# Optimization experiments

Measured on AMD Instinct MI355X. Metric: run time of the kernel, lower is better.

## Reference

```python
import jax, jax.numpy as jnp
from jax import lax
import numpy as np

# Quantization / layer config (mirrors QuantizedConv2d init_kwargs)
IN_ZP = 3
OUT_ZP = -2
IN_SCALE = 0.05
OUT_SCALE = 0.1
STRIDE = (1, 1)
PAD = (1, 1)  # (pad_h, pad_w)
DILATION = (1, 1)
GROUPS = 1
FEATURE_BITS = 8
Q_MIN, Q_MAX = -(1 << (FEATURE_BITS - 1)), (1 << (FEATURE_BITS - 1)) - 1  # -128, 127


def setup_inputs() -> dict:
    key = jax.random.key(0)
    k1, k2, k3, k4 = jax.random.split(key, 4)
    N, Cin, H, W = 32, 128, 56, 56
    Cout, KH, KW = 256, 3, 3
    x = jax.random.randint(k1, (N, Cin, H, W), -128, 128, dtype=jnp.int8)
    weight = jax.random.randint(k2, (Cout, Cin, KH, KW), -128, 128, dtype=jnp.int8)
    bias = jax.random.randint(k3, (Cout,), -1000, 1000, dtype=jnp.int32)  # shifted quantized bias
    weight_scale = jax.random.uniform(k4, (Cout,), dtype=jnp.float32, minval=1e-3, maxval=1e-2)
    return {"x": x, "weight": weight, "bias": bias, "weight_scale": weight_scale}


def reference(x, weight, bias, weight_scale):
    # q_y = round((CONV[q_x, q_w] + shifted_bias) * (S_x * S_w / S_y) + Z_y), clamped to int8
    # Pad with the input zero point (NOT zero), matching F.pad(..., value=input_zero_point)
    ph, pw = PAD
    xp = jnp.pad(x, ((0, 0), (0, 0), (ph, ph), (pw, pw)), constant_values=IN_ZP)
    # Exact integer convolution (matches the CPU int32 path; GPU float path rounds
    # back to the same int32 values)
    acc = lax.conv_general_dilated(
        xp.astype(jnp.int32), weight.astype(jnp.int32),
        window_strides=STRIDE, padding='VALID',
        rhs_dilation=DILATION, feature_group_count=GROUPS,
        dimension_numbers=('NCHW', 'OIHW', 'NCHW'))  # [N, Cout, H, W] int32
    acc = acc + bias[None, :, None, None]
    # Fused dequant/requant epilogue: per-channel scale, output zero point, round, clamp
    scale = (IN_SCALE * weight_scale / OUT_SCALE)[None, :, None, None]  # [1, Cout, 1, 1]
    y = acc.astype(jnp.float32) * scale + jnp.float32(OUT_ZP)
    return jnp.clip(jnp.round(y), Q_MIN, Q_MAX).astype(jnp.int8)
```

## Files before the change

### kernel.cpp

```cpp
#include <hip/hip_runtime.h>


#define NB    32
#define CIN   128
#define HH    56
#define WW    56
#define COUT  256
#define HP    58
#define WP    58
#define PIX   (HH*WW)
#define KTOT  1152
#define NCHUNK 18

#define NPT   28
#define BN    112
#define NJ    7
#define PHB1  (NJ*1024)

typedef int v4i __attribute__((ext_vector_type(4)));

#define GLOAD_LDS(gsrc, ldst) \
    __builtin_amdgcn_global_load_lds( \
        (const __attribute__((address_space(1))) void*)(gsrc), \
        (__attribute__((address_space(3))) void*)(ldst), 16, 0, 0)

__global__ void pack_both_kernel(const int* __restrict__ x,
                                 unsigned char* __restrict__ xp8,
                                 const int* __restrict__ wt,
                                 unsigned char* __restrict__ w8f,
                                 int n0) {
    __shared__ unsigned int lt[WW * 33];
    int bx = blockIdx.x;
    int tid = threadIdx.x;

    if (bx < COUT) {
        int co = bx;
        for (int idx = tid; idx < KTOT/4; idx += 256) {
            int k  = idx * 4;
            int r  = k >> 7;
            int ci = k & 127;
            const int* wb = wt + ((co*CIN + ci)*9 + r);
            int v0 = wb[0], v1 = wb[9], v2 = wb[18], v3 = wb[27];
            unsigned int pack = (v0 & 0xFF) | ((v1 & 0xFF) << 8) |
                                ((v2 & 0xFF) << 16) | ((unsigned)(v3 & 0xFF) << 24);
            int tch = k >> 6;
            size_t dst = ((size_t)((tch*16 + (co >> 4))*16 + (co & 15)))*64 + (k & 63);
            *(unsigned int*)(w8f + dst) = pack;
        }
        return;
    }

    int bxx = bx - COUT;
    int nl = bxx / HP;
    int hp = bxx % HP;
    int nb = n0 + nl;
    unsigned int* rowo = (unsigned int*)(xp8 + (size_t)(nl*HP + hp) * WP * CIN);

    if (hp == 0 || hp == HP-1) {
        const v4i zp = {0x03030303, 0x03030303, 0x03030303, 0x03030303};
        for (int i = tid; i < (WP*CIN)/16; i += 256)
            ((v4i*)rowo)[i] = zp;
        return;
    }

    int h  = hp - 1;
    int wl = tid & 63;
    int cg = tid >> 6;
    if (wl < WW) {
        const int s = HH*WW;
#pragma unroll
        for (int k = 0; k < 8; ++k) {
            int ci0 = cg*4 + k*16;
            const int* xb = x + (((size_t)(nb*CIN + ci0)*HH + h)*WW + wl);
            int v0 = xb[0], v1 = xb[s], v2 = xb[2*s], v3 = xb[3*s];
            unsigned int pack = (v0 & 0xFF) | ((v1 & 0xFF) << 8) |
                                ((v2 & 0xFF) << 16) | ((unsigned)(v3 & 0xFF) << 24);
            lt[wl*33 + (ci0 >> 2)] = pack;
        }
    }
    __syncthreads();

#pragma unroll
    for (int it = 0; it < 7; ++it) {
        int idx = it*256 + tid;
        int p = idx >> 5;
        int d = idx & 31;
        rowo[(p + 1)*32 + d] = lt[p*33 + d];
    }
    if (tid < 64) {
        int off = (tid < 32) ? tid : ((WP-1)*32 + (tid - 32));
        rowo[off] = 0x03030303u;
    }
}

__device__ __forceinline__ int koff_of(int t) {
    int r  = t >> 1;
    int kh = (r >= 6) ? 2 : (r >= 3 ? 1 : 0);
    int kw = r - kh*3;
    return ((kh*WP + kw) << 7) + ((t & 1) << 6);
}

__launch_bounds__(512, 4)
__global__ void conv_kernel(const unsigned char* __restrict__ w8f,
                            const unsigned char* __restrict__ xp8,
                            const int* __restrict__ bias,
                            const float* __restrict__ wscale,
                            int* __restrict__ out,
                            int n0) {
    __shared__ __align__(16) unsigned char ldsB[3*PHB1];

    int nwg = gridDim.x;
    int bx0 = blockIdx.x;
    int q = nwg >> 3, r = nwg & 7;
    int xcd = bx0 & 7, idx8 = bx0 >> 3;
    int bx = (xcd < r ? xcd*(q+1) : r*(q+1) + (xcd-r)*q) + idx8;

    int pt = bx % NPT;
    int nl = bx / NPT;
    int nb = n0 + nl;
    int p0 = pt * BN;

    int tid  = threadIdx.x;
    int lane = tid & 63;
    int wm   = tid >> 6;
    int lr   = lane & 15;
    int lg   = lane >> 4;

    int l4 = lane >> 2;
    int sw = (lane & 3) ^ ((lane >> 3) & 3);
    int slot = (wm < 7) ? wm : 6;
    int slotu = __builtin_amdgcn_readfirstlane(slot);
    int pS = p0 + slot*16 + l4;
    const unsigned char* bsrc =
        xp8 + ((size_t)((nl*HP + pS/WW)*WP + pS%WW))*CIN + sw*16;

    int rslot = lg ^ ((lr >> 1) & 3);
    int vb = lr*64 + rslot*16;

    const unsigned char* abase =
        w8f + (size_t)(wm*2)*1024 + (lr*64 + lg*16);

    v4i acc[2][NJ];
#pragma unroll
    for (int i = 0; i < 2; ++i)
#pragma unroll
        for (int j = 0; j < NJ; ++j)
            acc[i][j] = (v4i){0, 0, 0, 0};

#define STAGE1(T) \
    GLOAD_LDS(bsrc + koff_of(T), &ldsB[((T)%3)*PHB1 + slotu*1024])

    STAGE1(0);

#pragma unroll
    for (int p = 0; p < NCHUNK; ++p) {
        if (p < NCHUNK-1) STAGE1(p+1);

        v4i a_[2];
#pragma unroll
        for (int i = 0; i < 2; ++i)
            a_[i] = *(const v4i*)(abase + (size_t)p*16384 + i*1024);

        if (p == 0)             asm volatile("s_waitcnt vmcnt(3)" ::: "memory");
        else if (p == NCHUNK-1) asm volatile("s_waitcnt vmcnt(4)" ::: "memory");
        else                    asm volatile("s_waitcnt vmcnt(5)" ::: "memory");
        __builtin_amdgcn_sched_barrier(0);
        __builtin_amdgcn_s_barrier();

        int roff = (p % 3) * PHB1;
        v4i b_[NJ];
#pragma unroll
        for (int j = 0; j < NJ; ++j)
            b_[j] = *(const v4i*)&ldsB[roff + vb + j*1024];
#pragma unroll
        for (int i = 0; i < 2; ++i)
#pragma unroll
            for (int j = 0; j < NJ; ++j)
                acc[i][j] = __builtin_amdgcn_mfma_i32_16x16x64_i8(
                    a_[i], b_[j], acc[i][j], 0, 0, 0);
    }
#undef STAGE1

#pragma unroll
    for (int i = 0; i < 2; ++i) {
#pragma unroll
        for (int rr = 0; rr < 4; ++rr) {
            int co = wm*32 + i*16 + lg*4 + rr;
            float sc = __fdiv_rn(__fmul_rn(0.05f, wscale[co]), 0.1f);
            int bs = bias[co];
            int* orow = out + ((size_t)(nb*COUT + co))*PIX + p0;
#pragma unroll
            for (int j = 0; j < NJ; ++j) {
                float accf = (float)(acc[i][j][rr] + bs);
                float y = __fadd_rn(__fmul_rn(accf, sc), -2.0f);
                y = rintf(y);
                y = fminf(fmaxf(y, -128.0f), 127.0f);
                orow[j*16 + lr] = (int)y;
            }
        }
    }
}

__launch_bounds__(256)
__global__ void conv_direct_kernel(const int* __restrict__ x,
                                   const int* __restrict__ wt,
                                   const int* __restrict__ bias,
                                   const float* __restrict__ wscale,
                                   int* __restrict__ out) {
    size_t idx = (size_t)blockIdx.x * 256 + threadIdx.x;
    if (idx >= (size_t)NB * COUT * PIX) return;
    int w  = idx % WW;
    int h  = (idx / WW) % HH;
    int co = (idx / PIX) % COUT;
    int nb = idx / ((size_t)PIX * COUT);
    int acc = 0;
    for (int ci = 0; ci < CIN; ++ci) {
        const int* xb = x + ((size_t)(nb*CIN + ci)*HH)*WW;
        const int* wb = wt + ((size_t)(co*CIN + ci)*9);
        for (int kh = 0; kh < 3; ++kh) {
            int hh = h + kh - 1;
            for (int kw = 0; kw < 3; ++kw) {
                int ww2 = w + kw - 1;
                int xv = (hh >= 0 && hh < HH && ww2 >= 0 && ww2 < WW)
                         ? xb[hh*WW + ww2] : 3;
                acc += xv * wb[kh*3 + kw];
            }
        }
    }
    float sc = __fdiv_rn(__fmul_rn(0.05f, wscale[co]), 0.1f);
    float y = __fadd_rn(__fmul_rn((float)(acc + bias[co]), sc), -2.0f);
    y = rintf(y);
    y = fminf(fmaxf(y, -128.0f), 127.0f);
    out[idx] = (int)y;
}

extern "C" void kernel_launch(void* const* d_in, const int* in_sizes, int n_in,
                              void* d_out, int out_size, void* d_ws, size_t ws_size,
                              hipStream_t stream) {
    const int*   x      = (const int*)d_in[0];
    const int*   weight = (const int*)d_in[1];
    const int*   bias   = (const int*)d_in[2];
    const float* wscale = (const float*)d_in[3];
    int*         out    = (int*)d_out;

    const size_t XOFF = 320u << 10;
    const size_t BPB  = (size_t)HP * WP * CIN;
    const size_t SLAB = (size_t)COUT * PIX * 4;

    size_t navail = (ws_size > XOFF) ? (ws_size - XOFF) / BPB : 0;

    unsigned char* w8f = (unsigned char*)d_ws;
    unsigned char* xpw = (unsigned char*)d_ws + XOFF;

    if (navail >= 4) {
        int wsN = (int)(navail < 32 ? navail : 32);
        int Na  = 32 - wsN;
        unsigned char* xpt = (unsigned char*)d_out + (size_t)Na * SLAB;

        if (Na > 0) {
            pack_both_kernel<<<dim3(COUT + Na*HP), dim3(256), 0, stream>>>(
                x, xpt, weight, w8f, 0);
            pack_both_kernel<<<dim3(COUT + wsN*HP), dim3(256), 0, stream>>>(
                x, xpw, weight, w8f, Na);
            conv_kernel<<<dim3(NPT*Na), dim3(512), 0, stream>>>(
                w8f, xpt, bias, wscale, out, 0);
            conv_kernel<<<dim3(NPT*wsN), dim3(512), 0, stream>>>(
                w8f, xpw, bias, wscale, out, Na);
        } else {
            pack_both_kernel<<<dim3(COUT + 32*HP), dim3(256), 0, stream>>>(
                x, xpw, weight, w8f, 0);
            conv_kernel<<<dim3(NPT*32), dim3(512), 0, stream>>>(
                w8f, xpw, bias, wscale, out, 0);
        }
    } else if (navail >= 1) {
        int nchk = navail >= 2 ? 2 : 1;
        for (int n0 = 0; n0 < NB; n0 += nchk) {
            int nc = (NB - n0 < nchk) ? (NB - n0) : nchk;
            pack_both_kernel<<<dim3(COUT + nc*HP), dim3(256), 0, stream>>>(
                x, xpw, weight, w8f, n0);
            conv_kernel<<<dim3(NPT*nc), dim3(512), 0, stream>>>(
                w8f, xpw, bias, wscale, out, n0);
        }
    } else {
        size_t total = (size_t)NB * COUT * PIX;
        conv_direct_kernel<<<dim3((total + 255) / 256), dim3(256), 0, stream>>>(
            x, weight, bias, wscale, out);
    }
}
```

Before: 58.98 us.

## Split padded input into two 64-channel planes and reorder load/wait schedule

The packed padded input changes from one 128-byte-per-pixel NHWC layout to two separate 64-channel planes per image. Each K-chunk's global-to-LDS load now reads contiguous 64-byte pixels from a single plane, which may improve access locality. The main loop issues the weight register loads before the next-stage LDS prefetch, with adjusted waitcnt values. It also raises wave priority around the MFMA block. The risk is a wrong vmcnt ordering or a worse cache footprint, since a chunk now touches a different plane.

```diff
diff --git a/kernel.cpp b/kernel.cpp
--- a/kernel.cpp
+++ b/kernel.cpp
@@ -16,6 +16,8 @@
 #define BN    112
 #define NJ    7
 #define PHB1  (NJ*1024)
+#define PL    (HP*WP*64)
+#define BPB   (2*PL)
 
 typedef int v4i __attribute__((ext_vector_type(4)));
 
@@ -54,12 +56,15 @@
     int nl = bxx / HP;
     int hp = bxx % HP;
     int nb = n0 + nl;
-    unsigned int* rowo = (unsigned int*)(xp8 + (size_t)(nl*HP + hp) * WP * CIN);
+    unsigned char* slab = xp8 + (size_t)nl * BPB;
+    unsigned int* q0 = (unsigned int*)(slab + (size_t)hp * WP * 64);
+    unsigned int* q1 = (unsigned int*)(slab + PL + (size_t)hp * WP * 64);
 
     if (hp == 0 || hp == HP-1) {
         const v4i zp = {0x03030303, 0x03030303, 0x03030303, 0x03030303};
-        for (int i = tid; i < (WP*CIN)/16; i += 256)
-            ((v4i*)rowo)[i] = zp;
+        v4i* a0 = (v4i*)q0;
+        v4i* a1 = (v4i*)q1;
+        for (int i = tid; i < (WP*64)/16; i += 256) { a0[i] = zp; a1[i] = zp; }
         return;
     }
 
@@ -85,11 +90,14 @@
         int idx = it*256 + tid;
         int p = idx >> 5;
         int d = idx & 31;
-        rowo[(p + 1)*32 + d] = lt[p*33 + d];
+        unsigned int* qq = (d < 16) ? q0 : q1;
+        qq[(p + 1)*16 + (d & 15)] = lt[p*33 + d];
     }
     if (tid < 64) {
-        int off = (tid < 32) ? tid : ((WP-1)*32 + (tid - 32));
-        rowo[off] = 0x03030303u;
+        int d = tid & 15;
+        unsigned int* qq = (tid & 16) ? q1 : q0;
+        int col = (tid & 32) ? (WP-1) : 0;
+        qq[col*16 + d] = 0x03030303u;
     }
 }
 
@@ -97,7 +105,7 @@
     int r  = t >> 1;
     int kh = (r >= 6) ? 2 : (r >= 3 ? 1 : 0);
     int kw = r - kh*3;
-    return ((kh*WP + kw) << 7) + ((t & 1) << 6);
+    return (t & 1) * PL + ((kh*WP + kw) << 6);
 }
 
 __launch_bounds__(512, 4)
@@ -131,8 +139,9 @@
     int slot = (wm < 7) ? wm : 6;
     int slotu = __builtin_amdgcn_readfirstlane(slot);
     int pS = p0 + slot*16 + l4;
+    int ph = pS / WW, pw = pS % WW;
     const unsigned char* bsrc =
-        xp8 + ((size_t)((nl*HP + pS/WW)*WP + pS%WW))*CIN + sw*16;
+        xp8 + (size_t)nl*BPB + ((size_t)(ph*WP + pw))*64 + sw*16;
 
     int rslot = lg ^ ((lr >> 1) & 3);
     int vb = lr*64 + rslot*16;
@@ -154,16 +163,15 @@
 
 #pragma unroll
     for (int p = 0; p < NCHUNK; ++p) {
-        if (p < NCHUNK-1) STAGE1(p+1);
-
         v4i a_[2];
 #pragma unroll
         for (int i = 0; i < 2; ++i)
             a_[i] = *(const v4i*)(abase + (size_t)p*16384 + i*1024);
-
-        if (p == 0)             asm volatile("s_waitcnt vmcnt(3)" ::: "memory");
-        else if (p == NCHUNK-1) asm volatile("s_waitcnt vmcnt(4)" ::: "memory");
-        else                    asm volatile("s_waitcnt vmcnt(5)" ::: "memory");
+        __builtin_amdgcn_sched_barrier(0);
+        if (p < NCHUNK-1) STAGE1(p+1);
+
+        if (p < NCHUNK-1) asm volatile("s_waitcnt vmcnt(3)" ::: "memory");
+        else              asm volatile("s_waitcnt vmcnt(2)" ::: "memory");
         __builtin_amdgcn_sched_barrier(0);
         __builtin_amdgcn_s_barrier();
 
@@ -172,12 +180,14 @@
 #pragma unroll
         for (int j = 0; j < NJ; ++j)
             b_[j] = *(const v4i*)&ldsB[roff + vb + j*1024];
+        __builtin_amdgcn_s_setprio(1);
 #pragma unroll
         for (int i = 0; i < 2; ++i)
 #pragma unroll
             for (int j = 0; j < NJ; ++j)
                 acc[i][j] = __builtin_amdgcn_mfma_i32_16x16x64_i8(
                     a_[i], b_[j], acc[i][j], 0, 0, 0);
+        __builtin_amdgcn_s_setprio(0);
     }
 #undef STAGE1
 
@@ -244,7 +254,6 @@
     int*         out    = (int*)d_out;
 
     const size_t XOFF = 320u << 10;
-    const size_t BPB  = (size_t)HP * WP * CIN;
     const size_t SLAB = (size_t)COUT * PIX * 4;
 
     size_t navail = (ws_size > XOFF) ? (ws_size - XOFF) / BPB : 0;
```

Measured after the change: 58.10 us. About the same (-1.5%).
